# Kernel optimization log

Hardware: AMD Instinct MI355X
Metric: run time of the kernel (lower is better)

## Reference

```python
import jax, jax.numpy as jnp
import numpy as np

N_NODES = 50000
N_EDGES = 800000
D = 128
BN_EPS = 1e-5


def swish(h):
    return h * jax.nn.sigmoid(h)


def linear_bn_swish(h, W, b, g, be):
    # Linear -> BatchNorm1d (training stats, biased var) -> Swish
    h = h @ W + b
    mean = jnp.mean(h, axis=0)
    var = jnp.mean((h - mean) ** 2, axis=0)
    h = (h - mean) * jax.lax.rsqrt(var + BN_EPS) * g + be
    return swish(h)


def setup_inputs() -> dict:
    key = jax.random.key(0)
    ks = jax.random.split(key, 8)
    scale = 1.0 / np.sqrt(D)
    return {
        "x": jax.random.normal(ks[0], (N_NODES, D), dtype=jnp.float32),
        "vals": jax.random.uniform(ks[1], (N_EDGES,), dtype=jnp.float32),
        "W1": jax.random.normal(ks[2], (D, D), dtype=jnp.float32) * scale,
        "b1": jnp.zeros((D,), dtype=jnp.float32),
        "g1": jnp.ones((D,), dtype=jnp.float32),
        "be1": jnp.zeros((D,), dtype=jnp.float32),
        "W2": jax.random.normal(ks[3], (D, D), dtype=jnp.float32) * scale,
        "b2": jnp.zeros((D,), dtype=jnp.float32),
        "g2": jnp.ones((D,), dtype=jnp.float32),
        "be2": jnp.zeros((D,), dtype=jnp.float32),
        "eps": jnp.zeros((1,), dtype=jnp.float32),
        "rows": jax.random.randint(ks[4], (N_EDGES,), 0, N_NODES, dtype=jnp.int32),
        "cols": jax.random.randint(ks[5], (N_EDGES,), 0, N_NODES, dtype=jnp.int32),
    }


def reference(x, vals, W1, b1, g1, be1, W2, b2, g2, be2, eps, rows, cols):
    # out = spmm(adj, x): gather neighbor features, scale by edge weight, scatter-add to rows
    msgs = vals[:, None] * x[cols]                                   # [E, D]
    agg = jax.ops.segment_sum(msgs, rows, num_segments=x.shape[0])   # [N, D]
    h = agg + (1.0 + eps[0]) * x
    h = linear_bn_swish(h, W1, b1, g1, be1)
    h = linear_bn_swish(h, W2, b2, g2, be2)
    return h
```

## Files before the change

kernel.cpp:

```cpp
#include <hip/hip_runtime.h>

#define D 128
#define DH 64
#define BR 64
#define BSH 6
#define NBMAX 1024
#define FCAP 2048
#define GT 512

typedef float f32x4 __attribute__((ext_vector_type(4)));
typedef short s16x8 __attribute__((ext_vector_type(8)));

static __device__ __forceinline__ unsigned short f2bf(float f) {
    unsigned u = __float_as_uint(f);
    u += 0x7FFF + ((u >> 16) & 1);
    return (unsigned short)(u >> 16);
}
static __device__ __forceinline__ float bflo(unsigned u) { return __uint_as_float(u << 16); }
static __device__ __forceinline__ float bfhi(unsigned u) { return __uint_as_float(u & 0xFFFF0000u); }
static __device__ __forceinline__ float bf2f(short v) {
    return __uint_as_float(((unsigned)(unsigned short)v) << 16);
}

__global__ __launch_bounds__(256)
void k_setup(const float* __restrict__ x, unsigned* __restrict__ xh, int total4,
             const float* __restrict__ W1, const float* __restrict__ W2,
             unsigned short* __restrict__ Wsw1, unsigned short* __restrict__ Wsw2,
             int* __restrict__ ccur, float* __restrict__ stats, int eb) {
    int bid = blockIdx.x, t = threadIdx.x;
    if (bid < eb) {
        int i = bid * 256 + t;
        if (i < total4) {
            float4 v = ((const float4*)x)[i];
            uint2 o;
            o.x = (unsigned)f2bf(v.x) | ((unsigned)f2bf(v.y) << 16);
            o.y = (unsigned)f2bf(v.z) | ((unsigned)f2bf(v.w) << 16);
            ((uint2*)xh)[i] = o;
        }
    } else if (bid < eb + 16) {
        int gidx = (bid - eb) * 256 + t;
        const float* W = (gidx < 2048) ? W1 : W2;
        unsigned short* Wsw = (gidx < 2048) ? Wsw1 : Wsw2;
        int idx = gidx & 2047;
        int lane = idx & 63, nt = (idx >> 6) & 7, kt = idx >> 9;
        int k0 = kt * 32 + (lane >> 4) * 8;
        int n = nt * 16 + (lane & 15);
        unsigned short* dst = &Wsw[(size_t)((kt * 8 + nt) * 64 + lane) * 8];
#pragma unroll
        for (int j = 0; j < 8; ++j) dst[j] = f2bf(W[(k0 + j) * D + n]);
    } else {
        if (t < 512) stats[t] = 0.f;
        for (int i = t; i < NBMAX; i += 256) ccur[i] = 0;
    }
}

__global__ __launch_bounds__(256)
void k_cscatter(const int* __restrict__ rows, const int* __restrict__ cols,
                const float* __restrict__ vals, int* __restrict__ ccur,
                uint2* __restrict__ sedge, int E, int nb, int chunk) {
    __shared__ int lcnt[NBMAX];
    __shared__ int lbase[NBMAX];
    int t = threadIdx.x;
    int c0 = blockIdx.x * chunk;
    int c1 = min(c0 + chunk, E);
    if (c0 >= E) return;
    for (int i = t; i < nb; i += 256) lcnt[i] = 0;
    __syncthreads();
    for (int e = c0 + t; e < c1; e += 256)
        atomicAdd(&lcnt[rows[e] >> BSH], 1);
    __syncthreads();
    for (int i = t; i < nb; i += 256) {
        int c = lcnt[i];
        lbase[i] = c ? atomicAdd(&ccur[i], c) : 0;
        lcnt[i] = 0;
    }
    __syncthreads();
    for (int e = c0 + t; e < c1; e += 256) {
        int r = rows[e];
        int b = r >> BSH;
        int rk = atomicAdd(&lcnt[b], 1);
        int pos = lbase[b] + rk;
        uint2 ed;
        ed.x = (unsigned)cols[e] | ((unsigned)(r & (BR - 1)) << 16);
        ed.y = __float_as_uint(vals[e]);
        if (pos < FCAP) sedge[(size_t)b * FCAP + pos] = ed;
    }
}

__global__ __launch_bounds__(GT, 8)
void k_sortgather(const uint2* __restrict__ sedge, const int* __restrict__ ccur,
                  const unsigned* __restrict__ xh, const float* __restrict__ eps,
                  unsigned* __restrict__ aggh, int N) {
    __shared__ int cnt[BR], sbase[BR], cur[BR];
    __shared__ uint2 ebufA[FCAP];
    __shared__ uint2 ebufB[FCAP];
    int b = blockIdx.x, t = threadIdx.x;
    size_t e0 = (size_t)b * FCAP;
    int cntE = ccur[b];
    if (cntE > FCAP) cntE = FCAP;
    if (t < BR) { cnt[t] = 0; cur[t] = 0; }
    __syncthreads();
    for (int i = t; i < cntE; i += GT) {
        uint2 ed = sedge[e0 + i];
        ebufA[i] = ed;
        atomicAdd(&cnt[ed.x >> 16], 1);
    }
    __syncthreads();
    if (t < BR) sbase[t] = cnt[t];
    __syncthreads();
    for (int d = 1; d < BR; d <<= 1) {
        int add = (t < BR && t >= d) ? sbase[t - d] : 0;
        __syncthreads();
        if (t < BR) sbase[t] += add;
        __syncthreads();
    }
    if (t < BR) sbase[t] -= cnt[t];
    __syncthreads();
    for (int i = t; i < cntE; i += GT) {
        uint2 ed = ebufA[i];
        int r = ed.x >> 16;
        int p = sbase[r] + atomicAdd(&cur[r], 1);
        ebufB[p] = make_uint2(ed.x & 0xFFFFu, ed.y);
    }
    __syncthreads();

    int lane = t & 63, w = t >> 6;
    float s = 1.0f + eps[0];
    int row0 = b * BR;
    for (int rl = w; rl < BR; rl += 8) {
        int grow = row0 + rl;
        if (grow >= N) break;
        unsigned u = xh[(size_t)grow * DH + lane];
        float ax = s * bflo(u), ay = s * bfhi(u);
        int i = sbase[rl];
        int i1 = (rl < BR - 1) ? sbase[rl + 1] : cntE;
        for (; i + 8 <= i1; i += 8) {
            uint2 ed[8];
            unsigned uu[8];
#pragma unroll
            for (int j = 0; j < 8; ++j) ed[j] = ebufB[i + j];
#pragma unroll
            for (int j = 0; j < 8; ++j) uu[j] = xh[(size_t)ed[j].x * DH + lane];
#pragma unroll
            for (int j = 0; j < 8; ++j) {
                float v = __uint_as_float(ed[j].y);
                ax += v * bflo(uu[j]);
                ay += v * bfhi(uu[j]);
            }
        }
        for (; i < i1; ++i) {
            uint2 ed = ebufB[i];
            unsigned uu = xh[(size_t)ed.x * DH + lane];
            float v = __uint_as_float(ed.y);
            ax += v * bflo(uu);
            ay += v * bfhi(uu);
        }
        aggh[(size_t)grow * DH + lane] = (unsigned)f2bf(ax) | ((unsigned)f2bf(ay) << 16);
    }
}

__global__ __launch_bounds__(256)
void k_gemm(const unsigned short* __restrict__ A, const unsigned short* __restrict__ Wsw,
            const float* __restrict__ bias, unsigned short* __restrict__ Hout,
            float* __restrict__ stats, int N) {
    __shared__ float redS[4 * D];
    __shared__ float redQ[4 * D];
    int tid = threadIdx.x, lane = tid & 63, w = tid >> 6;
    int row0 = blockIdx.x * 64 + w * 16;
    int m = lane & 15, quad = lane >> 4;

    f32x4 acc[8];
#pragma unroll
    for (int nt = 0; nt < 8; ++nt) acc[nt] = (f32x4){0.f, 0.f, 0.f, 0.f};

    int arow = row0 + m;
    bool avalid = arow < N;
    const s16x8* wp = (const s16x8*)Wsw;
    s16x8 az = {0, 0, 0, 0, 0, 0, 0, 0};
#pragma unroll
    for (int kt = 0; kt < 4; ++kt) {
        s16x8 a = avalid ? *(const s16x8*)&A[(size_t)arow * D + kt * 32 + quad * 8] : az;
#pragma unroll
        for (int nt = 0; nt < 8; ++nt) {
            s16x8 b = wp[(kt * 8 + nt) * 64 + lane];
            acc[nt] = __builtin_amdgcn_mfma_f32_16x16x32_bf16(a, b, acc[nt], 0, 0, 0);
        }
    }

#pragma unroll
    for (int nt = 0; nt < 8; ++nt) {
        float bv = bias[nt * 16 + m];
        float s = 0.f, q = 0.f;
#pragma unroll
        for (int r = 0; r < 4; ++r) {
            int row = row0 + quad * 4 + r;
            float h = acc[nt][r] + bv;
            if (row < N) {
                Hout[(size_t)row * D + nt * 16 + m] = f2bf(h);
                s += h; q += h * h;
            }
        }
        s += __shfl_xor(s, 16, 64); s += __shfl_xor(s, 32, 64);
        q += __shfl_xor(q, 16, 64); q += __shfl_xor(q, 32, 64);
        if (quad == 0) {
            redS[w * D + nt * 16 + m] = s;
            redQ[w * D + nt * 16 + m] = q;
        }
    }
    __syncthreads();
    if (tid < D) {
        float ts = redS[tid] + redS[D + tid] + redS[2 * D + tid] + redS[3 * D + tid];
        float tq = redQ[tid] + redQ[D + tid] + redQ[2 * D + tid] + redQ[3 * D + tid];
        atomicAdd(&stats[tid], ts);
        atomicAdd(&stats[D + tid], tq);
    }
}

__global__ __launch_bounds__(256)
void k_gemm2f(const unsigned short* __restrict__ H1, const unsigned short* __restrict__ Wsw,
              const float* __restrict__ bias, const float* __restrict__ stats1,
              const float* __restrict__ g1, const float* __restrict__ be1, float invN,
              unsigned short* __restrict__ Hout, float* __restrict__ stats2, int N) {
    __shared__ float redS[4 * D];
    __shared__ float redQ[4 * D];
    __shared__ float sa[D], sb[D];
    int tid = threadIdx.x, lane = tid & 63, w = tid >> 6;
    if (tid < D) {
        float mean = stats1[tid] * invN;
        float var = fmaxf(stats1[D + tid] * invN - mean * mean, 0.f);
        float a = g1[tid] * rsqrtf(var + 1e-5f);
        sa[tid] = a;
        sb[tid] = be1[tid] - mean * a;
    }
    __syncthreads();

    int row0 = blockIdx.x * 64 + w * 16;
    int m = lane & 15, quad = lane >> 4;

    f32x4 acc[8];
#pragma unroll
    for (int nt = 0; nt < 8; ++nt) acc[nt] = (f32x4){0.f, 0.f, 0.f, 0.f};

    int arow = row0 + m;
    bool avalid = arow < N;
    const s16x8* wp = (const s16x8*)Wsw;
    s16x8 az = {0, 0, 0, 0, 0, 0, 0, 0};
#pragma unroll
    for (int kt = 0; kt < 4; ++kt) {
        s16x8 a = az;
        if (avalid) {
            s16x8 raw = *(const s16x8*)&H1[(size_t)arow * D + kt * 32 + quad * 8];
#pragma unroll
            for (int j = 0; j < 8; ++j) {
                int k = kt * 32 + quad * 8 + j;
                float dd = bf2f(raw[j]) * sa[k] + sb[k];
                float o = dd / (1.f + __expf(-dd));
                a[j] = (short)f2bf(o);
            }
        }
#pragma unroll
        for (int nt = 0; nt < 8; ++nt) {
            s16x8 b = wp[(kt * 8 + nt) * 64 + lane];
            acc[nt] = __builtin_amdgcn_mfma_f32_16x16x32_bf16(a, b, acc[nt], 0, 0, 0);
        }
    }

#pragma unroll
    for (int nt = 0; nt < 8; ++nt) {
        float bv = bias[nt * 16 + m];
        float s = 0.f, q = 0.f;
#pragma unroll
        for (int r = 0; r < 4; ++r) {
            int row = row0 + quad * 4 + r;
            float h = acc[nt][r] + bv;
            if (row < N) {
                Hout[(size_t)row * D + nt * 16 + m] = f2bf(h);
                s += h; q += h * h;
            }
        }
        s += __shfl_xor(s, 16, 64); s += __shfl_xor(s, 32, 64);
        q += __shfl_xor(q, 16, 64); q += __shfl_xor(q, 32, 64);
        if (quad == 0) {
            redS[w * D + nt * 16 + m] = s;
            redQ[w * D + nt * 16 + m] = q;
        }
    }
    __syncthreads();
    if (tid < D) {
        float ts = redS[tid] + redS[D + tid] + redS[2 * D + tid] + redS[3 * D + tid];
        float tq = redQ[tid] + redQ[D + tid] + redQ[2 * D + tid] + redQ[3 * D + tid];
        atomicAdd(&stats2[tid], ts);
        atomicAdd(&stats2[D + tid], tq);
    }
}

__global__ void k_bnswish(const unsigned* __restrict__ inh, float* __restrict__ outp,
                          const float* __restrict__ stats, const float* __restrict__ g,
                          const float* __restrict__ be, float invN, int total4) {
    __shared__ float sa[D], sb[D];
    int j = threadIdx.x;
    if (j < D) {
        float mean = stats[j] * invN;
        float var = fmaxf(stats[D + j] * invN - mean * mean, 0.f);
        float a = g[j] * rsqrtf(var + 1e-5f);
        sa[j] = a;
        sb[j] = be[j] - mean * a;
    }
    __syncthreads();
    int i = blockIdx.x * blockDim.x + threadIdx.x;
    if (i >= total4) return;
    uint2 u = ((const uint2*)inh)[i];
    int c = (i * 4) & (D - 1);
    float d0 = bflo(u.x) * sa[c + 0] + sb[c + 0];
    float d1 = bfhi(u.x) * sa[c + 1] + sb[c + 1];
    float d2 = bflo(u.y) * sa[c + 2] + sb[c + 2];
    float d3 = bfhi(u.y) * sa[c + 3] + sb[c + 3];
    float o0 = d0 / (1.f + __expf(-d0));
    float o1 = d1 / (1.f + __expf(-d1));
    float o2 = d2 / (1.f + __expf(-d2));
    float o3 = d3 / (1.f + __expf(-d3));
    ((float4*)outp)[i] = make_float4(o0, o1, o2, o3);
}

extern "C" void kernel_launch(void* const* d_in, const int* in_sizes, int n_in,
                              void* d_out, int out_size, void* d_ws, size_t ws_size,
                              hipStream_t stream) {
    const float* x    = (const float*)d_in[0];
    const float* vals = (const float*)d_in[1];
    const float* W1   = (const float*)d_in[2];
    const float* b1   = (const float*)d_in[3];
    const float* g1   = (const float*)d_in[4];
    const float* be1  = (const float*)d_in[5];
    const float* W2   = (const float*)d_in[6];
    const float* b2   = (const float*)d_in[7];
    const float* g2   = (const float*)d_in[8];
    const float* be2  = (const float*)d_in[9];
    const float* eps  = (const float*)d_in[10];
    const int*  rows  = (const int*)d_in[11];
    const int*  cols  = (const int*)d_in[12];
    float* out = (float*)d_out;

    int N = in_sizes[0] / D;
    int E = in_sizes[1];
    int nb = (N + BR - 1) / BR;

    char* p = (char*)d_ws;
    float* stats = (float*)p;              p += 4 * D * sizeof(float);
    int* ccur = (int*)p;                   p += (size_t)NBMAX * sizeof(int);
    p = (char*)(((uintptr_t)p + 15) & ~(uintptr_t)15);
    unsigned short* Wsw1 = (unsigned short*)p; p += (size_t)D * D * 2;
    unsigned short* Wsw2 = (unsigned short*)p; p += (size_t)D * D * 2;
    p = (char*)(((uintptr_t)p + 15) & ~(uintptr_t)15);
    uint2* sedge  = (uint2*)p;             p += (size_t)nb * FCAP * sizeof(uint2);
    unsigned* xh = (unsigned*)p;           p += (size_t)N * DH * sizeof(unsigned);
    unsigned* aggh = (unsigned*)p;

    float* stats1 = stats;
    float* stats2 = stats + 2 * D;

    int total4 = N * D / 4;
    int eb = (total4 + 255) / 256;
    int gblk = (N + 63) / 64;
    int chunk = (E + 255) / 256;
    float invN = 1.0f / (float)N;

    k_setup<<<eb + 17, 256, 0, stream>>>(x, xh, total4, W1, W2, Wsw1, Wsw2,
                                         ccur, stats, eb);
    k_cscatter<<<256, 256, 0, stream>>>(rows, cols, vals, ccur, sedge, E, nb, chunk);
    k_sortgather<<<nb, GT, 0, stream>>>(sedge, ccur, xh, eps, aggh, N);
    k_gemm<<<gblk, 256, 0, stream>>>((const unsigned short*)aggh, Wsw1, b1,
                                     (unsigned short*)xh, stats1, N);
    k_gemm2f<<<gblk, 256, 0, stream>>>((const unsigned short*)xh, Wsw2, b2,
                                       stats1, g1, be1, invN,
                                       (unsigned short*)aggh, stats2, N);
    k_bnswish<<<eb, 256, 0, stream>>>(aggh, out, stats2, g2, be2, invN, total4);
}
```

Measured before the change: 236.4 us.

## Replace block bucket sort with per-row slabs and fuse gather into first GEMM

Drops the two-level block bucketing and in-LDS counting sort, and replaces them with a direct per-row atomic scatter into fixed-capacity row slabs (64 edges per row). The neighbour gather now writes its bf16 aggregate into a shared-memory tile that feeds the first MFMA GEMM in the same kernel, so the aggregate no longer round-trips through global memory and one launch disappears. The trade is one global atomic per edge on a 50k-entry counter array and a larger, sparsely filled slab buffer. Rows with more than 64 edges are silently truncated. Separate h1/h2 buffers replace the reuse of xh, which the first GEMM now reads.

```diff
diff --git a/kernel.cpp b/kernel.cpp
--- a/kernel.cpp
+++ b/kernel.cpp
@@ -2,11 +2,8 @@
 
 #define D 128
 #define DH 64
-#define BR 64
-#define BSH 6
-#define NBMAX 1024
-#define FCAP 2048
-#define GT 512
+#define RCAP 64
+#define TS 68
 
 typedef float f32x4 __attribute__((ext_vector_type(4)));
 typedef short s16x8 __attribute__((ext_vector_type(8)));
@@ -26,7 +23,7 @@
 void k_setup(const float* __restrict__ x, unsigned* __restrict__ xh, int total4,
              const float* __restrict__ W1, const float* __restrict__ W2,
              unsigned short* __restrict__ Wsw1, unsigned short* __restrict__ Wsw2,
-             int* __restrict__ ccur, float* __restrict__ stats, int eb) {
+             int* __restrict__ rowcnt, float* __restrict__ stats, int eb, int npad) {
     int bid = blockIdx.x, t = threadIdx.x;
     if (bid < eb) {
         int i = bid * 256 + t;
@@ -49,96 +46,53 @@
 #pragma unroll
         for (int j = 0; j < 8; ++j) dst[j] = f2bf(W[(k0 + j) * D + n]);
     } else {
-        if (t < 512) stats[t] = 0.f;
-        for (int i = t; i < NBMAX; i += 256) ccur[i] = 0;
+        int z = bid - eb - 16;
+        int idx = z * 256 + t;
+        if (idx < npad) rowcnt[idx] = 0;
+        if (z == 0) { stats[t] = 0.f; stats[256 + t] = 0.f; }
     }
 }
 
 __global__ __launch_bounds__(256)
-void k_cscatter(const int* __restrict__ rows, const int* __restrict__ cols,
-                const float* __restrict__ vals, int* __restrict__ ccur,
-                uint2* __restrict__ sedge, int E, int nb, int chunk) {
-    __shared__ int lcnt[NBMAX];
-    __shared__ int lbase[NBMAX];
-    int t = threadIdx.x;
-    int c0 = blockIdx.x * chunk;
-    int c1 = min(c0 + chunk, E);
-    if (c0 >= E) return;
-    for (int i = t; i < nb; i += 256) lcnt[i] = 0;
-    __syncthreads();
-    for (int e = c0 + t; e < c1; e += 256)
-        atomicAdd(&lcnt[rows[e] >> BSH], 1);
-    __syncthreads();
-    for (int i = t; i < nb; i += 256) {
-        int c = lcnt[i];
-        lbase[i] = c ? atomicAdd(&ccur[i], c) : 0;
-        lcnt[i] = 0;
-    }
-    __syncthreads();
-    for (int e = c0 + t; e < c1; e += 256) {
+void k_scatter(const int* __restrict__ rows, const int* __restrict__ cols,
+               const float* __restrict__ vals, int* __restrict__ rowcnt,
+               uint2* __restrict__ rowslab, int E) {
+    int stride = gridDim.x * blockDim.x;
+    for (int e = blockIdx.x * blockDim.x + threadIdx.x; e < E; e += stride) {
         int r = rows[e];
-        int b = r >> BSH;
-        int rk = atomicAdd(&lcnt[b], 1);
-        int pos = lbase[b] + rk;
-        uint2 ed;
-        ed.x = (unsigned)cols[e] | ((unsigned)(r & (BR - 1)) << 16);
-        ed.y = __float_as_uint(vals[e]);
-        if (pos < FCAP) sedge[(size_t)b * FCAP + pos] = ed;
-    }
-}
-
-__global__ __launch_bounds__(GT, 8)
-void k_sortgather(const uint2* __restrict__ sedge, const int* __restrict__ ccur,
-                  const unsigned* __restrict__ xh, const float* __restrict__ eps,
-                  unsigned* __restrict__ aggh, int N) {
-    __shared__ int cnt[BR], sbase[BR], cur[BR];
-    __shared__ uint2 ebufA[FCAP];
-    __shared__ uint2 ebufB[FCAP];
-    int b = blockIdx.x, t = threadIdx.x;
-    size_t e0 = (size_t)b * FCAP;
-    int cntE = ccur[b];
-    if (cntE > FCAP) cntE = FCAP;
-    if (t < BR) { cnt[t] = 0; cur[t] = 0; }
-    __syncthreads();
-    for (int i = t; i < cntE; i += GT) {
-        uint2 ed = sedge[e0 + i];
-        ebufA[i] = ed;
-        atomicAdd(&cnt[ed.x >> 16], 1);
-    }
-    __syncthreads();
-    if (t < BR) sbase[t] = cnt[t];
-    __syncthreads();
-    for (int d = 1; d < BR; d <<= 1) {
-        int add = (t < BR && t >= d) ? sbase[t - d] : 0;
-        __syncthreads();
-        if (t < BR) sbase[t] += add;
-        __syncthreads();
-    }
-    if (t < BR) sbase[t] -= cnt[t];
-    __syncthreads();
-    for (int i = t; i < cntE; i += GT) {
-        uint2 ed = ebufA[i];
-        int r = ed.x >> 16;
-        int p = sbase[r] + atomicAdd(&cur[r], 1);
-        ebufB[p] = make_uint2(ed.x & 0xFFFFu, ed.y);
-    }
-    __syncthreads();
-
-    int lane = t & 63, w = t >> 6;
+        int p = atomicAdd(&rowcnt[r], 1);
+        if (p < RCAP)
+            rowslab[(size_t)r * RCAP + p] =
+                make_uint2((unsigned)cols[e], __float_as_uint(vals[e]));
+    }
+}
+
+__global__ __launch_bounds__(256)
+void k_gathergemm1(const uint2* __restrict__ rowslab, const int* __restrict__ rowcnt,
+                   const unsigned* __restrict__ xh, const float* __restrict__ eps,
+                   const unsigned short* __restrict__ Wsw, const float* __restrict__ bias,
+                   unsigned short* __restrict__ Hout, float* __restrict__ stats, int N) {
+    __shared__ unsigned tile[64 * TS];
+    __shared__ float redS[4 * D];
+    __shared__ float redQ[4 * D];
+    int tid = threadIdx.x, lane = tid & 63, w = tid >> 6;
+    int row0 = blockIdx.x * 64;
     float s = 1.0f + eps[0];
-    int row0 = b * BR;
-    for (int rl = w; rl < BR; rl += 8) {
+
+    for (int rl = w; rl < 64; rl += 4) {
         int grow = row0 + rl;
-        if (grow >= N) break;
+        if (grow >= N) { tile[rl * TS + lane] = 0; continue; }
         unsigned u = xh[(size_t)grow * DH + lane];
         float ax = s * bflo(u), ay = s * bfhi(u);
-        int i = sbase[rl];
-        int i1 = (rl < BR - 1) ? sbase[rl + 1] : cntE;
-        for (; i + 8 <= i1; i += 8) {
+        int cnt = rowcnt[grow];
+        if (cnt > RCAP) cnt = RCAP;
+        const uint2* base = &rowslab[(size_t)grow * RCAP];
+        int i = 0;
+        for (; i + 8 <= cnt; i += 8) {
             uint2 ed[8];
             unsigned uu[8];
 #pragma unroll
-            for (int j = 0; j < 8; ++j) ed[j] = ebufB[i + j];
+            for (int j = 0; j < 8; ++j) ed[j] = base[i + j];
 #pragma unroll
             for (int j = 0; j < 8; ++j) uu[j] = xh[(size_t)ed[j].x * DH + lane];
 #pragma unroll
@@ -148,38 +102,28 @@
                 ay += v * bfhi(uu[j]);
             }
         }
-        for (; i < i1; ++i) {
-            uint2 ed = ebufB[i];
+        for (; i < cnt; ++i) {
+            uint2 ed = base[i];
             unsigned uu = xh[(size_t)ed.x * DH + lane];
             float v = __uint_as_float(ed.y);
             ax += v * bflo(uu);
             ay += v * bfhi(uu);
         }
-        aggh[(size_t)grow * DH + lane] = (unsigned)f2bf(ax) | ((unsigned)f2bf(ay) << 16);
-    }
-}
-
-__global__ __launch_bounds__(256)
-void k_gemm(const unsigned short* __restrict__ A, const unsigned short* __restrict__ Wsw,
-            const float* __restrict__ bias, unsigned short* __restrict__ Hout,
-            float* __restrict__ stats, int N) {
-    __shared__ float redS[4 * D];
-    __shared__ float redQ[4 * D];
-    int tid = threadIdx.x, lane = tid & 63, w = tid >> 6;
-    int row0 = blockIdx.x * 64 + w * 16;
+        tile[rl * TS + lane] = (unsigned)f2bf(ax) | ((unsigned)f2bf(ay) << 16);
+    }
+    __syncthreads();
+
     int m = lane & 15, quad = lane >> 4;
+    int wrow0 = row0 + w * 16;
 
     f32x4 acc[8];
 #pragma unroll
     for (int nt = 0; nt < 8; ++nt) acc[nt] = (f32x4){0.f, 0.f, 0.f, 0.f};
 
-    int arow = row0 + m;
-    bool avalid = arow < N;
     const s16x8* wp = (const s16x8*)Wsw;
-    s16x8 az = {0, 0, 0, 0, 0, 0, 0, 0};
 #pragma unroll
     for (int kt = 0; kt < 4; ++kt) {
-        s16x8 a = avalid ? *(const s16x8*)&A[(size_t)arow * D + kt * 32 + quad * 8] : az;
+        s16x8 a = *(const s16x8*)&tile[(w * 16 + m) * TS + kt * 16 + quad * 4];
 #pragma unroll
         for (int nt = 0; nt < 8; ++nt) {
             s16x8 b = wp[(kt * 8 + nt) * 64 + lane];
@@ -190,20 +134,20 @@
 #pragma unroll
     for (int nt = 0; nt < 8; ++nt) {
         float bv = bias[nt * 16 + m];
-        float s = 0.f, q = 0.f;
+        float ss = 0.f, q = 0.f;
 #pragma unroll
         for (int r = 0; r < 4; ++r) {
-            int row = row0 + quad * 4 + r;
+            int row = wrow0 + quad * 4 + r;
             float h = acc[nt][r] + bv;
             if (row < N) {
                 Hout[(size_t)row * D + nt * 16 + m] = f2bf(h);
-                s += h; q += h * h;
+                ss += h; q += h * h;
             }
         }
-        s += __shfl_xor(s, 16, 64); s += __shfl_xor(s, 32, 64);
-        q += __shfl_xor(q, 16, 64); q += __shfl_xor(q, 32, 64);
+        ss += __shfl_xor(ss, 16, 64); ss += __shfl_xor(ss, 32, 64);
+        q += __shfl_xor(q, 16, 64);   q += __shfl_xor(q, 32, 64);
         if (quad == 0) {
-            redS[w * D + nt * 16 + m] = s;
+            redS[w * D + nt * 16 + m] = ss;
             redQ[w * D + nt * 16 + m] = q;
         }
     }
@@ -342,36 +286,36 @@
 
     int N = in_sizes[0] / D;
     int E = in_sizes[1];
-    int nb = (N + BR - 1) / BR;
+    int gblk = (N + 63) / 64;
+    int npad = gblk * 64;
 
     char* p = (char*)d_ws;
     float* stats = (float*)p;              p += 4 * D * sizeof(float);
-    int* ccur = (int*)p;                   p += (size_t)NBMAX * sizeof(int);
+    int* rowcnt = (int*)p;                 p += (size_t)npad * sizeof(int);
     p = (char*)(((uintptr_t)p + 15) & ~(uintptr_t)15);
     unsigned short* Wsw1 = (unsigned short*)p; p += (size_t)D * D * 2;
     unsigned short* Wsw2 = (unsigned short*)p; p += (size_t)D * D * 2;
     p = (char*)(((uintptr_t)p + 15) & ~(uintptr_t)15);
-    uint2* sedge  = (uint2*)p;             p += (size_t)nb * FCAP * sizeof(uint2);
+    uint2* rowslab = (uint2*)p;            p += (size_t)npad * RCAP * sizeof(uint2);
     unsigned* xh = (unsigned*)p;           p += (size_t)N * DH * sizeof(unsigned);
-    unsigned* aggh = (unsigned*)p;
+    unsigned* h1 = (unsigned*)p;           p += (size_t)N * DH * sizeof(unsigned);
+    unsigned* h2 = (unsigned*)p;
 
     float* stats1 = stats;
     float* stats2 = stats + 2 * D;
 
     int total4 = N * D / 4;
     int eb = (total4 + 255) / 256;
-    int gblk = (N + 63) / 64;
-    int chunk = (E + 255) / 256;
+    int zb = (npad + 255) / 256;
     float invN = 1.0f / (float)N;
 
-    k_setup<<<eb + 17, 256, 0, stream>>>(x, xh, total4, W1, W2, Wsw1, Wsw2,
-                                         ccur, stats, eb);
-    k_cscatter<<<256, 256, 0, stream>>>(rows, cols, vals, ccur, sedge, E, nb, chunk);
-    k_sortgather<<<nb, GT, 0, stream>>>(sedge, ccur, xh, eps, aggh, N);
-    k_gemm<<<gblk, 256, 0, stream>>>((const unsigned short*)aggh, Wsw1, b1,
-                                     (unsigned short*)xh, stats1, N);
-    k_gemm2f<<<gblk, 256, 0, stream>>>((const unsigned short*)xh, Wsw2, b2,
+    k_setup<<<eb + 16 + zb, 256, 0, stream>>>(x, xh, total4, W1, W2, Wsw1, Wsw2,
+                                              rowcnt, stats, eb, npad);
+    k_scatter<<<1024, 256, 0, stream>>>(rows, cols, vals, rowcnt, rowslab, E);
+    k_gathergemm1<<<gblk, 256, 0, stream>>>(rowslab, rowcnt, xh, eps, Wsw1, b1,
+                                            (unsigned short*)h1, stats1, N);
+    k_gemm2f<<<gblk, 256, 0, stream>>>((const unsigned short*)h1, Wsw2, b2,
                                        stats1, g1, be1, invN,
-                                       (unsigned short*)aggh, stats2, N);
-    k_bnswish<<<eb, 256, 0, stream>>>(aggh, out, stats2, g2, be2, invN, total4);
-}
+                                       (unsigned short*)h2, stats2, N);
+    k_bnswish<<<eb, 256, 0, stream>>>(h2, out, stats2, g2, be2, invN, total4);
+}
```

New measurement: 277.7 us. +17.5%, slower.

## Stage edge buckets in LDS before scattering to global bucket slots

Applied to the files above, without the earlier changes.

The edge bucketing kernel now processes fixed 4096-edge chunks with 512 threads, loads each edge once into registers, and computes local bucket offsets with a shared-memory prefix scan. Edges are locally sorted into LDS by bucket and then written out in bucket order, so global stores to the same bucket are contiguous rather than scattered. This replaces the older scheme that read rows twice and wrote each edge to a random location. In exchange it adds a 10-step scan with barriers, more LDS use (about 52KB), and roughly 196 blocks instead of 256.

```diff
diff --git a/kernel.cpp b/kernel.cpp
--- a/kernel.cpp
+++ b/kernel.cpp
@@ -7,6 +7,8 @@
 #define NBMAX 1024
 #define FCAP 2048
 #define GT 512
+#define CH 4096
+#define SCT 512
 
 typedef float f32x4 __attribute__((ext_vector_type(4)));
 typedef short s16x8 __attribute__((ext_vector_type(8)));
@@ -54,36 +56,77 @@
     }
 }
 
-__global__ __launch_bounds__(256)
+__global__ __launch_bounds__(SCT)
 void k_cscatter(const int* __restrict__ rows, const int* __restrict__ cols,
-                const float* __restrict__ vals, int* __restrict__ ccur,
-                uint2* __restrict__ sedge, int E, int nb, int chunk) {
+                const float* __restrict__ vals, int* __restrict__ gcur,
+                uint2* __restrict__ sedge, int E) {
     __shared__ int lcnt[NBMAX];
     __shared__ int lbase[NBMAX];
+    __shared__ int gbase[NBMAX];
+    __shared__ uint2 sl[CH];
+    __shared__ unsigned short sbkt[CH];
     int t = threadIdx.x;
-    int c0 = blockIdx.x * chunk;
-    int c1 = min(c0 + chunk, E);
-    if (c0 >= E) return;
-    for (int i = t; i < nb; i += 256) lcnt[i] = 0;
-    __syncthreads();
-    for (int e = c0 + t; e < c1; e += 256)
-        atomicAdd(&lcnt[rows[e] >> BSH], 1);
-    __syncthreads();
-    for (int i = t; i < nb; i += 256) {
-        int c = lcnt[i];
-        lbase[i] = c ? atomicAdd(&ccur[i], c) : 0;
-        lcnt[i] = 0;
-    }
-    __syncthreads();
-    for (int e = c0 + t; e < c1; e += 256) {
-        int r = rows[e];
-        int b = r >> BSH;
-        int rk = atomicAdd(&lcnt[b], 1);
-        int pos = lbase[b] + rk;
-        uint2 ed;
-        ed.x = (unsigned)cols[e] | ((unsigned)(r & (BR - 1)) << 16);
-        ed.y = __float_as_uint(vals[e]);
-        if (pos < FCAP) sedge[(size_t)b * FCAP + pos] = ed;
+    int base = blockIdx.x * CH;
+    int tot = min(E - base, CH);
+
+    for (int i = t; i < NBMAX; i += SCT) lcnt[i] = 0;
+    __syncthreads();
+
+    int r[8]; unsigned c[8], v[8];
+#pragma unroll
+    for (int j = 0; j < 8; ++j) {
+        int e = base + j * SCT + t;
+        if (e < E) {
+            r[j] = rows[e];
+            c[j] = (unsigned)cols[e];
+            v[j] = __float_as_uint(vals[e]);
+            atomicAdd(&lcnt[r[j] >> BSH], 1);
+        } else r[j] = -1;
+    }
+    __syncthreads();
+
+    lbase[t] = lcnt[t];
+    lbase[t + SCT] = lcnt[t + SCT];
+    __syncthreads();
+    for (int d = 1; d < NBMAX; d <<= 1) {
+        int a0 = (t >= d) ? lbase[t - d] : 0;
+        int i1 = t + SCT;
+        int a1 = (i1 >= d) ? lbase[i1 - d] : 0;
+        __syncthreads();
+        lbase[t] += a0;
+        lbase[i1] += a1;
+        __syncthreads();
+    }
+#pragma unroll
+    for (int k = 0; k < 2; ++k) {
+        int i = t + k * SCT;
+        int cnt = lcnt[i];
+        gbase[i] = cnt ? atomicAdd(&gcur[i], cnt) : 0;
+        lbase[i] -= cnt;
+    }
+    __syncthreads();
+    for (int i = t; i < NBMAX; i += SCT) lcnt[i] = 0;
+    __syncthreads();
+
+#pragma unroll
+    for (int j = 0; j < 8; ++j) {
+        if (r[j] >= 0) {
+            int b = r[j] >> BSH;
+            int p = lbase[b] + atomicAdd(&lcnt[b], 1);
+            sl[p] = make_uint2(c[j] | ((unsigned)(r[j] & (BR - 1)) << 16), v[j]);
+            sbkt[p] = (unsigned short)b;
+        }
+    }
+    __syncthreads();
+
+#pragma unroll
+    for (int j = 0; j < 8; ++j) {
+        int i = j * SCT + t;
+        if (i < tot) {
+            int b = sbkt[i];
+            int pos = gbase[b] + (i - lbase[b]);
+            if (pos < FCAP) sedge[(size_t)b * FCAP + pos] = sl[i];
+        }
     }
 }
 
@@ -361,12 +404,12 @@
     int total4 = N * D / 4;
     int eb = (total4 + 255) / 256;
     int gblk = (N + 63) / 64;
-    int chunk = (E + 255) / 256;
     float invN = 1.0f / (float)N;
+    int scb = (E + CH - 1) / CH;
 
     k_setup<<<eb + 17, 256, 0, stream>>>(x, xh, total4, W1, W2, Wsw1, Wsw2,
                                          ccur, stats, eb);
-    k_cscatter<<<256, 256, 0, stream>>>(rows, cols, vals, ccur, sedge, E, nb, chunk);
+    k_cscatter<<<scb, SCT, 0, stream>>>(rows, cols, vals, ccur, sedge, E);
     k_sortgather<<<nb, GT, 0, stream>>>(sedge, ccur, xh, eps, aggh, N);
     k_gemm<<<gblk, 256, 0, stream>>>((const unsigned short*)aggh, Wsw1, b1,
                                      (unsigned short*)xh, stats1, N);
```

After: 221.8 us. 6.2% less time.
